# Kernel optimization log

Hardware: AMD Instinct MI355X
Metric: run time of the kernel (lower is better)

Reference implementation:

```python
import jax, jax.numpy as jnp
import numpy as np

Q_CHAN = 8          # q_chan
IN_CHAN = 128
KS = 56             # kernel_size; ks*ks must equal h*w
STRIDE = 2
BN_EPS = 1e-5


def setup_inputs() -> dict:
    key = jax.random.key(0)
    ks = jax.random.split(key, 10)
    n, c, h, w = 4, IN_CHAN, 56, 56
    hw = h * w  # 3136 == KS*KS
    oc = 4 * Q_CHAN  # qkv conv output channels = 32
    return {
        "x": jax.random.normal(ks[0], (n, c, h, w), dtype=jnp.float32),
        # 1x1 conv weight (out_ch, in_ch) and bias
        "w_qkv": jax.random.normal(ks[1], (oc, c), dtype=jnp.float32) * (1.0 / np.sqrt(c)),
        "b_qkv": jnp.zeros((oc,), dtype=jnp.float32),
        # BatchNorm (inference mode) affine + running stats
        "bn_gamma": jnp.ones((oc,), dtype=jnp.float32),
        "bn_beta": jnp.zeros((oc,), dtype=jnp.float32),
        "bn_mean": jnp.zeros((oc,), dtype=jnp.float32),
        "bn_var": jnp.ones((oc,), dtype=jnp.float32),
        # learned relative position biases, trailing dim = ks*ks = h*w
        "rq": jax.random.normal(ks[2], (Q_CHAN, KS * KS), dtype=jnp.float32),
        "rk": jax.random.normal(ks[3], (Q_CHAN, KS * KS), dtype=jnp.float32),
        "rv": jax.random.normal(ks[4], (2 * Q_CHAN, KS * KS), dtype=jnp.float32),
    }


def reference(x, w_qkv, b_qkv, bn_gamma, bn_beta, bn_mean, bn_var, rq, rk, rv):
    n, c, h, w = x.shape
    # 1x1 conv + inference BatchNorm
    qkv = jnp.einsum('nchw,oc->nohw', x, w_qkv) + b_qkv[None, :, None, None]
    scale = bn_gamma / jnp.sqrt(bn_var + BN_EPS)
    qkv = (qkv - bn_mean[None, :, None, None]) * scale[None, :, None, None] + bn_beta[None, :, None, None]
    qkv = qkv.reshape(n, 4 * Q_CHAN, h * w)
    q = qkv[:, :Q_CHAN]            # [n, 8, hw]
    k = qkv[:, Q_CHAN:2 * Q_CHAN]  # [n, 8, hw]
    v = qkv[:, 2 * Q_CHAN:]        # [n, 16, hw]
    # global attention scores with learned positional bias terms: [n, hw, hw]
    sc = (jnp.einsum('nci,ncj->nij', q, k)
          + jnp.einsum('ci,ncj->nij', rq, q)
          + jnp.einsum('ci,ncj->nij', rk, k))
    sc = jax.nn.softmax(sc, axis=2)
    v = v + rv[None]
    out = jnp.einsum('nij,ncj->nci', sc, v).reshape(n, 2 * Q_CHAN, h, w)
    # AvgPool2d(kernel=stride, stride=stride)
    s = STRIDE
    out = out.reshape(n, 2 * Q_CHAN, h // s, s, w // s, s).mean(axis=(3, 5))
    return out
```

## Files before the change

### kernel.cpp

```cpp
#include <hip/hip_runtime.h>

#define HW 3136
#define CIN 128
#define MHAT 40.0f
#define NSEV 7
#define LOG2E 1.44269504088896340736f
#define NEGC  (-57.7078018f)

typedef __attribute__((ext_vector_type(8))) short bf16x8;
typedef __attribute__((ext_vector_type(4))) float f32x4;

__device__ __forceinline__ unsigned cvtpk(float a, float b) {
    unsigned r;
    asm("v_cvt_pk_bf16_f32 %0, %1, %2" : "=v"(r) : "v"(a), "v"(b));
    return r;
}
__device__ __forceinline__ float lo2f(unsigned p) { return __uint_as_float(p << 16); }
__device__ __forceinline__ float hi2f(unsigned p) { return __uint_as_float(p & 0xffff0000u); }
__device__ __forceinline__ float exp2_hw(float x) {
    float r;
    asm("v_exp_f32 %0, %1" : "=v"(r) : "v"(x));
    return r;
}
__device__ __forceinline__ void pl32(unsigned &a, unsigned &b) {
    asm("v_permlane32_swap_b32 %0, %1" : "+v"(a), "+v"(b));
}
__device__ __forceinline__ void pl16(unsigned &a, unsigned &b) {
    asm("v_permlane16_swap_b32 %0, %1" : "+v"(a), "+v"(b));
}

union UF { bf16x8 v; unsigned u[4]; };


__global__ __launch_bounds__(64) void proj_mfma(
    const float* __restrict__ x, const float* __restrict__ w,
    const float* __restrict__ bq, const float* __restrict__ gm,
    const float* __restrict__ bt, const float* __restrict__ mu,
    const float* __restrict__ vr, const float* __restrict__ rq,
    const float* __restrict__ rk, const float* __restrict__ rv,
    short* __restrict__ QKWS, short* __restrict__ ASQB, short* __restrict__ VWS)
{
    const int lane = threadIdx.x;
    const int il = lane & 15, q = lane >> 4;
    const int jb = blockIdx.x * 16;
    const int nn = blockIdx.y;
    const int jA = jb + il;
    const float* xn = x + (size_t)nn * CIN * HW;

    UF xh[4], xl[4];
    #pragma unroll
    for (int s = 0; s < 4; ++s) {
        float xv[8];
        #pragma unroll
        for (int u = 0; u < 8; ++u)
            xv[u] = xn[(size_t)(s * 32 + q * 8 + u) * HW + jA];
        #pragma unroll
        for (int t = 0; t < 4; ++t) {
            unsigned hp = cvtpk(xv[2 * t], xv[2 * t + 1]);
            unsigned lp = cvtpk(xv[2 * t] - lo2f(hp), xv[2 * t + 1] - hi2f(hp));
            xh[s].u[t] = hp;
            xl[s].u[t] = lp;
        }
    }
    UF wh0[4], wl0[4], wh1[4], wl1[4];
    {
        const float* wp0 = w + (size_t)il * CIN;
        const float* wp1 = w + (size_t)(16 + il) * CIN;
        #pragma unroll
        for (int s = 0; s < 4; ++s) {
            float4 f0 = *(const float4*)(wp0 + s * 32 + q * 8);
            float4 f1 = *(const float4*)(wp0 + s * 32 + q * 8 + 4);
            float g0[8] = {f0.x, f0.y, f0.z, f0.w, f1.x, f1.y, f1.z, f1.w};
            float4 h0 = *(const float4*)(wp1 + s * 32 + q * 8);
            float4 h1 = *(const float4*)(wp1 + s * 32 + q * 8 + 4);
            float g1[8] = {h0.x, h0.y, h0.z, h0.w, h1.x, h1.y, h1.z, h1.w};
            #pragma unroll
            for (int t = 0; t < 4; ++t) {
                unsigned hp0 = cvtpk(g0[2 * t], g0[2 * t + 1]);
                unsigned lp0 = cvtpk(g0[2 * t] - lo2f(hp0), g0[2 * t + 1] - hi2f(hp0));
                wh0[s].u[t] = hp0;
                wl0[s].u[t] = lp0;
                unsigned hp1 = cvtpk(g1[2 * t], g1[2 * t + 1]);
                unsigned lp1 = cvtpk(g1[2 * t] - lo2f(hp1), g1[2 * t + 1] - hi2f(hp1));
                wh1[s].u[t] = hp1;
                wl1[s].u[t] = lp1;
            }
        }
    }

    f32x4 a0 = {0.f, 0.f, 0.f, 0.f}, a1 = {0.f, 0.f, 0.f, 0.f};
    #pragma unroll
    for (int s = 0; s < 4; ++s) a0 = __builtin_amdgcn_mfma_f32_16x16x32_bf16(wh0[s].v, xh[s].v, a0, 0, 0, 0);
    #pragma unroll
    for (int s = 0; s < 4; ++s) a1 = __builtin_amdgcn_mfma_f32_16x16x32_bf16(wl0[s].v, xh[s].v, a1, 0, 0, 0);
    #pragma unroll
    for (int s = 0; s < 4; ++s) a1 = __builtin_amdgcn_mfma_f32_16x16x32_bf16(wh0[s].v, xl[s].v, a1, 0, 0, 0);
    const f32x4 d0 = a0 + a1;
    f32x4 b0 = {0.f, 0.f, 0.f, 0.f}, b1 = {0.f, 0.f, 0.f, 0.f};
    #pragma unroll
    for (int s = 0; s < 4; ++s) b0 = __builtin_amdgcn_mfma_f32_16x16x32_bf16(xh[s].v, wh1[s].v, b0, 0, 0, 0);
    #pragma unroll
    for (int s = 0; s < 4; ++s) b1 = __builtin_amdgcn_mfma_f32_16x16x32_bf16(xl[s].v, wh1[s].v, b1, 0, 0, 0);
    #pragma unroll
    for (int s = 0; s < 4; ++s) b1 = __builtin_amdgcn_mfma_f32_16x16x32_bf16(xh[s].v, wl1[s].v, b1, 0, 0, 0);
    const f32x4 d1 = b0 + b1;

    {
        const int jj = jA;
        float hv[4], av[4];
        #pragma unroll
        for (int r = 0; r < 4; ++r) {
            const int ch = q * 4 + r;
            const float sc = gm[ch] * rsqrtf(vr[ch] + 1e-5f);
            const float sh = (bq[ch] - mu[ch]) * sc + bt[ch];
            const float val = d0[r] * sc + sh;
            hv[r] = val;
            const float a = (ch < 8) ? (val + rk[(size_t)ch * HW + jj])
                                     : rq[(size_t)(ch - 8) * HW + jj];
            av[r] = a * LOG2E;
        }
        short* qrow = QKWS + ((size_t)nn * HW + jj) * 32;
        short* arow = ASQB + ((size_t)nn * HW + jj) * 32;
        const int pb = (q * 4) ^ 8;
        unsigned h01 = cvtpk(hv[0], hv[1]), h23 = cvtpk(hv[2], hv[3]);
        unsigned l01 = cvtpk(hv[0] - lo2f(h01), hv[1] - hi2f(h01));
        unsigned l23 = cvtpk(hv[2] - lo2f(h23), hv[3] - hi2f(h23));
        *(unsigned*)&qrow[pb]          = h01;
        *(unsigned*)&qrow[pb + 2]      = h23;
        *(unsigned*)&qrow[16 + pb]     = l01;
        *(unsigned*)&qrow[16 + pb + 2] = l23;
        unsigned c01 = cvtpk(av[0], av[1]), c23 = cvtpk(av[2], av[3]);
        unsigned e01 = cvtpk(av[0] - lo2f(c01), av[1] - hi2f(c01));
        unsigned e23 = cvtpk(av[2] - lo2f(c23), av[3] - hi2f(c23));
        *(unsigned*)&arow[q * 4]          = c01;
        *(unsigned*)&arow[q * 4 + 2]      = c23;
        *(unsigned*)&arow[16 + q * 4]     = e01;
        *(unsigned*)&arow[16 + q * 4 + 2] = e23;
    }
    {
        const int ch = 16 + il;
        const float sc = gm[ch] * rsqrtf(vr[ch] + 1e-5f);
        const float sh = (bq[ch] - mu[ch]) * sc + bt[ch];
        const int jbase = jb + q * 4;
        float4 rvv = *(const float4*)(rv + (size_t)il * HW + jbase);
        float v0 = d1[0] * sc + sh + rvv.x;
        float v1 = d1[1] * sc + sh + rvv.y;
        float v2 = d1[2] * sc + sh + rvv.z;
        float v3 = d1[3] * sc + sh + rvv.w;
        short* vp = VWS + (size_t)(nn * 16 + il) * HW + jbase;
        *(unsigned*)&vp[0] = cvtpk(v0, v1);
        *(unsigned*)&vp[2] = cvtpk(v2, v3);
    }
}

#define JT 224
#define QKS 40
#define VTS 232

__global__ __launch_bounds__(256) void attn_mfma(
    const short* __restrict__ QKWS, const short* __restrict__ ASQB,
    const short* __restrict__ VWS,
    float* __restrict__ ONUM, float* __restrict__ OLS)
{
    __shared__ short QK[JT * QKS + 16];
    __shared__ short VT[16 * VTS];
    const int tid = threadIdx.x;
    const int wv = tid >> 6, lane = tid & 63;
    const int il = lane & 15, q = lane >> 4;
    const int b   = blockIdx.x;
    const int sev = b / 196;
    const int ig  = b % 196;
    const int nn  = ig / 49;
    const int tile = (ig % 49) * 4 + wv;
    const int i0  = tile * 16;

    const bf16x8 bco = *(const bf16x8*)(ASQB + ((size_t)nn * HW + i0 + il) * 32 + q * 8);

    const f32x4 DINIT = {NEGC, NEGC, NEGC, NEGC};
    f32x4 outc = {0.f, 0.f, 0.f, 0.f};
    float lsum = 0.f;

    const int jb0 = (sev * 2 + 0) * JT;
    const int jb1 = (sev * 2 + 1) * JT;
    const int c_v = tid >> 4, jg = tid & 15;

    int4 qa0, qa1, qa2, qa3;
    unsigned vt0, vt1, vt2, vt3, vt4, vt5, vt6;

    if (tid < 8) ((unsigned*)(QK + JT * QKS))[tid] = 0u;

    if (tid < JT) {
        const short* src = QKWS + ((size_t)nn * HW + jb0 + tid) * 32;
        qa0 = *(const int4*)(src);
        qa1 = *(const int4*)(src + 8);
        qa2 = *(const int4*)(src + 16);
        qa3 = *(const int4*)(src + 24);
    }
    {
        const unsigned* vs = (const unsigned*)(VWS + (size_t)(nn * 16 + c_v) * HW + jb0 + jg * 14);
        vt0 = vs[0]; vt1 = vs[1]; vt2 = vs[2]; vt3 = vs[3]; vt4 = vs[4]; vt5 = vs[5]; vt6 = vs[6];
    }
    if (tid < JT) {
        short* row = &QK[tid * QKS];
        *(int4*)&row[0]  = qa0;
        *(int4*)&row[8]  = qa1;
        *(int4*)&row[16] = qa2;
        *(int4*)&row[24] = qa3;
    }
    {
        unsigned* vd = (unsigned*)&VT[c_v * VTS + jg * 14];
        vd[0] = vt0; vd[1] = vt1; vd[2] = vt2; vd[3] = vt3; vd[4] = vt4; vd[5] = vt5; vd[6] = vt6;
    }
    __syncthreads();

    if (tid < JT) {
        const short* src = QKWS + ((size_t)nn * HW + jb1 + tid) * 32;
        qa0 = *(const int4*)(src);
        qa1 = *(const int4*)(src + 8);
        qa2 = *(const int4*)(src + 16);
        qa3 = *(const int4*)(src + 24);
    }
    {
        const unsigned* vs = (const unsigned*)(VWS + (size_t)(nn * 16 + c_v) * HW + jb1 + jg * 14);
        vt0 = vs[0]; vt1 = vs[1]; vt2 = vs[2]; vt3 = vs[3]; vt4 = vs[4]; vt5 = vs[5]; vt6 = vs[6];
    }

    auto compute7 = [&]() {
        const short* zrow = &QK[JT * QKS];
        #pragma unroll
        for (int pr = 0; pr < 7; ++pr) {
            unsigned E0, E1, O0, O1;
            {
                const short* arow = &QK[((2 * pr) * 16 + il) * QKS + (q & 1) * 8];
                bf16x8 a1 = *(const bf16x8*)arow;
                bf16x8 a2 = *(const bf16x8*)((lane < 32) ? arow + 16 : zrow);
                __builtin_amdgcn_s_setprio(1);
                f32x4 d = __builtin_amdgcn_mfma_f32_16x16x32_bf16(a1, bco, DINIT, 0, 0, 0);
                d = __builtin_amdgcn_mfma_f32_16x16x32_bf16(a2, bco, d, 0, 0, 0);
                __builtin_amdgcn_s_setprio(0);
                float p0 = exp2_hw(d[0]), p1 = exp2_hw(d[1]);
                float p2 = exp2_hw(d[2]), p3 = exp2_hw(d[3]);
                lsum += (p0 + p1) + (p2 + p3);
                E0 = cvtpk(p0, p1); E1 = cvtpk(p2, p3);
            }
            {
                const short* arow = &QK[((2 * pr + 1) * 16 + il) * QKS + (q & 1) * 8];
                bf16x8 a1 = *(const bf16x8*)arow;
                bf16x8 a2 = *(const bf16x8*)((lane < 32) ? arow + 16 : zrow);
                __builtin_amdgcn_s_setprio(1);
                f32x4 d = __builtin_amdgcn_mfma_f32_16x16x32_bf16(a1, bco, DINIT, 0, 0, 0);
                d = __builtin_amdgcn_mfma_f32_16x16x32_bf16(a2, bco, d, 0, 0, 0);
                __builtin_amdgcn_s_setprio(0);
                float p0 = exp2_hw(d[0]), p1 = exp2_hw(d[1]);
                float p2 = exp2_hw(d[2]), p3 = exp2_hw(d[3]);
                lsum += (p0 + p1) + (p2 + p3);
                O0 = cvtpk(p0, p1); O1 = cvtpk(p2, p3);
            }
            pl32(E0, O0); pl32(E1, O1);
            pl16(E0, O0); pl16(E1, O1);
            UF ap; ap.u[0] = E0; ap.u[1] = E1; ap.u[2] = O0; ap.u[3] = O1;
            bf16x8 bv = *(const bf16x8*)&VT[il * VTS + pr * 32 + q * 8];
            __builtin_amdgcn_s_setprio(1);
            outc = __builtin_amdgcn_mfma_f32_16x16x32_bf16(ap.v, bv, outc, 0, 0, 0);
            __builtin_amdgcn_s_setprio(0);
        }
    };

    compute7();
    __syncthreads();

    if (tid < JT) {
        short* row = &QK[tid * QKS];
        *(int4*)&row[0]  = qa0;
        *(int4*)&row[8]  = qa1;
        *(int4*)&row[16] = qa2;
        *(int4*)&row[24] = qa3;
    }
    {
        unsigned* vd = (unsigned*)&VT[c_v * VTS + jg * 14];
        vd[0] = vt0; vd[1] = vt1; vd[2] = vt2; vd[3] = vt3; vd[4] = vt4; vd[5] = vt5; vd[6] = vt6;
    }
    __syncthreads();

    compute7();

    lsum += __shfl_xor(lsum, 16);
    lsum += __shfl_xor(lsum, 32);
    float* np = ONUM + ((size_t)(sev * 4 + nn) * 196 + tile) * 256;
    *(f32x4*)(np + il * 16 + q * 4) = outc;
    if (lane < 16)
        OLS[(size_t)(sev * 4 + nn) * HW + i0 + lane] = lsum;
}

__global__ __launch_bounds__(256) void pool_kernel(
    const float* __restrict__ ONUM, const float* __restrict__ OLS,
    float* __restrict__ out)
{
    __shared__ float LI[112];
    __shared__ float PL[2][16][28];
    const int tid = threadIdx.x;
    const int oh  = blockIdx.x;
    const int nn  = blockIdx.y;
    const int T0  = 7 * oh;

    if (tid < 112) {
        float l = 0.f;
        #pragma unroll
        for (int p = 0; p < NSEV; ++p)
            l += OLS[(size_t)(p * 4 + nn) * HW + 112 * oh + tid];
        LI[tid] = l;
    }
    __syncthreads();

    const int c  = tid >> 4;
    const int u0 = tid & 15;
    for (int u = u0; u < 28; u += 16) {
        const int tt = u >> 2, qd = u & 3;
        const int o  = u * 4;
        float4 nu = {0.f, 0.f, 0.f, 0.f};
        #pragma unroll
        for (int p = 0; p < NSEV; ++p) {
            const float4 v = *(const float4*)(ONUM +
                ((size_t)(p * 4 + nn) * 196 + T0 + tt) * 256 + c * 16 + qd * 4);
            nu.x += v.x; nu.y += v.y; nu.z += v.z; nu.w += v.w;
        }
        const float r0 = nu.x / LI[o], r1 = nu.y / LI[o + 1];
        const float r2 = nu.z / LI[o + 2], r3 = nu.w / LI[o + 3];
        const int hb = o / 56, wo = o % 56;
        PL[hb][c][wo >> 1]       = r0 + r1;
        PL[hb][c][(wo >> 1) + 1] = r2 + r3;
    }
    __syncthreads();

    for (int v = tid; v < 448; v += 256) {
        const int cc = v / 28, wo = v % 28;
        out[((nn * 16 + cc) * 28 + oh) * 28 + wo] = 0.25f * (PL[0][cc][wo] + PL[1][cc][wo]);
    }
}

#define FJC 392
#define FPSTR 394

__global__ __launch_bounds__(512, 2) void fused_attn(
    const float* __restrict__ x, const float* __restrict__ w,
    const float* __restrict__ bq, const float* __restrict__ gm,
    const float* __restrict__ bt, const float* __restrict__ mu,
    const float* __restrict__ vr, const float* __restrict__ rq,
    const float* __restrict__ rk, const float* __restrict__ rv,
    float* __restrict__ out)
{
    __shared__ float PT[32][FPSTR];
    __shared__ float SQ[56][16];
    __shared__ float ST[56][17];

    const int tid  = threadIdx.x;
    const int wv   = tid >> 6, lane = tid & 63;
    const int bid  = blockIdx.x;
    const int nn   = bid / 56, rem = bid % 56;
    const int oh   = rem >> 1, half = rem & 1;
    const float* xn = x + (size_t)nn * CIN * HW;

    if (tid < 448) {
        int r = tid >> 3, c = tid & 7;
        int rh = (r >= 28) ? 1 : 0, rw = r - 28*rh;
        int i  = (2*oh + rh)*56 + half*28 + rw;
        float acc = 0.f;
        for (int cc = 0; cc < CIN; ++cc)
            acc += xn[cc*HW + i] * w[c*CIN + cc];
        float s  = gm[c] * rsqrtf(vr[c] + 1e-5f);
        float qv = (acc + bq[c] - mu[c])*s + bt[c];
        SQ[r][c]   = qv + rk[c*HW + i];
        SQ[r][8+c] = rq[c*HW + i];
    }

    float l_[7];
    float ac_[7][16];
    #pragma unroll
    for (int r = 0; r < 7; ++r) {
        l_[r] = 0.f;
        #pragma unroll
        for (int c = 0; c < 16; ++c) ac_[r][c] = 0.f;
    }
    __syncthreads();

    for (int cb = 0; cb < 8; ++cb) {
        const int jbase = cb * FJC;
        const int o0 = wv * 4;
        for (int t = 0; t < 4; ++t) {
            int p = lane + 64*t;
            if (p < 196) {
                int j0 = jbase + 2*p;
                float a0x=0.f,a0y=0.f,a1x=0.f,a1y=0.f,a2x=0.f,a2y=0.f,a3x=0.f,a3y=0.f;
                for (int cc = 0; cc < CIN; ++cc) {
                    float2 xv = *(const float2*)(xn + (size_t)cc*HW + j0);
                    float w0 = w[(o0+0)*CIN + cc];
                    float w1 = w[(o0+1)*CIN + cc];
                    float w2 = w[(o0+2)*CIN + cc];
                    float w3 = w[(o0+3)*CIN + cc];
                    a0x += xv.x*w0; a0y += xv.y*w0;
                    a1x += xv.x*w1; a1y += xv.y*w1;
                    a2x += xv.x*w2; a2y += xv.y*w2;
                    a3x += xv.x*w3; a3y += xv.y*w3;
                }
                #pragma unroll
                for (int u = 0; u < 4; ++u) {
                    int o = o0 + u;
                    float av0 = (u==0)? a0x : (u==1)? a1x : (u==2)? a2x : a3x;
                    float av1 = (u==0)? a0y : (u==1)? a1y : (u==2)? a2y : a3y;
                    float s  = gm[o] * rsqrtf(vr[o] + 1e-5f);
                    float sh = (bq[o] - mu[o])*s + bt[o];
                    float v0 = av0*s + sh, v1 = av1*s + sh;
                    if (o >= 16) {
                        v0 += rv[(o-16)*HW + j0];
                        v1 += rv[(o-16)*HW + j0 + 1];
                    }
                    *(float2*)&PT[o][2*p] = make_float2(v0, v1);
                }
            }
        }
        __syncthreads();

        #pragma unroll
        for (int rr = 0; rr < 7; rr += 2) {
            const bool two = (rr + 1) < 7;
            const int ra = wv*7 + rr;
            float A1a[8], A2a[8], A1b[8], A2b[8];
            #pragma unroll
            for (int c = 0; c < 8; ++c) {
                A1a[c] = SQ[ra][c];   A2a[c] = SQ[ra][8+c];
                A1b[c] = two ? SQ[ra+1][c]   : 0.f;
                A2b[c] = two ? SQ[ra+1][8+c] : 0.f;
            }
            for (int t = 0; t < 7; ++t) {
                int jl = 64*t + lane;
                if (jl < FJC) {
                    float qv[8], kv[8], vv[16];
                    #pragma unroll
                    for (int c = 0; c < 8; ++c) { qv[c] = PT[c][jl]; kv[c] = PT[8+c][jl]; }
                    #pragma unroll
                    for (int c = 0; c < 16; ++c) vv[c] = PT[16+c][jl];
                    float sa = 0.f, sb = 0.f;
                    #pragma unroll
                    for (int c = 0; c < 8; ++c) {
                        sa += A1a[c]*kv[c] + A2a[c]*qv[c];
                        sb += A1b[c]*kv[c] + A2b[c]*qv[c];
                    }
                    float pa = __expf(sa - MHAT);
                    l_[rr] += pa;
                    #pragma unroll
                    for (int c = 0; c < 16; ++c) ac_[rr][c] += pa * vv[c];
                    if (two) {
                        float pb = __expf(sb - MHAT);
                        l_[rr+1] += pb;
                        #pragma unroll
                        for (int c = 0; c < 16; ++c) ac_[rr+1][c] += pb * vv[c];
                    }
                }
            }
        }
        __syncthreads();
    }

    #pragma unroll
    for (int rr = 0; rr < 7; ++rr) {
        int r = wv*7 + rr;
        float l = l_[rr];
        #pragma unroll
        for (int off = 32; off; off >>= 1) l += __shfl_xor(l, off);
        if (lane == 0) ST[r][16] = l;
        #pragma unroll
        for (int c = 0; c < 16; ++c) {
            float a = ac_[rr][c];
            #pragma unroll
            for (int off = 32; off; off >>= 1) a += __shfl_xor(a, off);
            if (lane == c) ST[r][c] = a;
        }
    }
    __syncthreads();

    if (tid < 224) {
        int c = tid & 15, qq = tid >> 4;
        float s = 0.f;
        #pragma unroll
        for (int rh = 0; rh < 2; ++rh)
            #pragma unroll
            for (int dw = 0; dw < 2; ++dw) {
                int r = rh*28 + 2*qq + dw;
                s += ST[r][c] / ST[r][16];
            }
        out[((nn*16 + c)*28 + oh)*28 + half*14 + qq] = 0.25f * s;
    }
}

extern "C" void kernel_launch(void* const* d_in, const int* in_sizes, int n_in,
                              void* d_out, int out_size, void* d_ws, size_t ws_size,
                              hipStream_t stream) {
    const float* x     = (const float*)d_in[0];
    const float* w     = (const float*)d_in[1];
    const float* bq    = (const float*)d_in[2];
    const float* gm    = (const float*)d_in[3];
    const float* bt    = (const float*)d_in[4];
    const float* mu    = (const float*)d_in[5];
    const float* vr    = (const float*)d_in[6];
    const float* rq    = (const float*)d_in[7];
    const float* rk    = (const float*)d_in[8];
    const float* rv    = (const float*)d_in[9];
    float* out = (float*)d_out;

    const size_t ONF = (size_t)NSEV * 4 * 196 * 256;
    const size_t OLF = (size_t)NSEV * 4 * HW;
    const size_t QKF = (size_t)4 * HW * 32;
    const size_t VWF = (size_t)4 * 16 * HW;
    const size_t NEED = (ONF + OLF) * sizeof(float) + (2 * QKF + VWF) * sizeof(short);

    if (ws_size >= NEED) {
        float* ONUM = (float*)d_ws;
        float* OLS  = ONUM + ONF;
        short* QKWS = (short*)(OLS + OLF);
        short* ASQB = QKWS + QKF;
        short* VWS  = ASQB + QKF;
        proj_mfma<<<dim3(196, 4), 64, 0, stream>>>(x, w, bq, gm, bt, mu, vr, rq, rk, rv, QKWS, ASQB, VWS);
        attn_mfma<<<dim3(196 * NSEV), 256, 0, stream>>>(QKWS, ASQB, VWS, ONUM, OLS);
        pool_kernel<<<dim3(28, 4), 256, 0, stream>>>(ONUM, OLS, out);
    } else {
        fused_attn<<<dim3(224), dim3(512), 0, stream>>>(x, w, bq, gm, bt, mu, vr, rq, rk, rv, out);
    }
}
```

Baseline: 97.57 us.

## Split projection K-reduction across two waves and zero B operand instead of LDS zero row

The projection kernel now runs two waves per block, each handling half of the 128-channel reduction, and combines their partial sums through shared memory before one wave writes QK/ASQB and the other writes V. This aims to cut per-wave load latency and register pressure in the memory-bound projection stage. In the attention kernel, the second score MFMA now zeroes the B operand for the upper lanes instead of steering those lanes to a zero row in LDS. That removes a per-iteration select and the zero-row init, at the cost of one extra register vector.

```diff
diff --git a/kernel.cpp b/kernel.cpp
--- a/kernel.cpp
+++ b/kernel.cpp
@@ -32,7 +32,7 @@
 union UF { bf16x8 v; unsigned u[4]; };
 
 
-__global__ __launch_bounds__(64) void proj_mfma(
+__global__ __launch_bounds__(128) void proj_mfma(
     const float* __restrict__ x, const float* __restrict__ w,
     const float* __restrict__ bq, const float* __restrict__ gm,
     const float* __restrict__ bt, const float* __restrict__ mu,
@@ -40,34 +40,40 @@
     const float* __restrict__ rk, const float* __restrict__ rv,
     short* __restrict__ QKWS, short* __restrict__ ASQB, short* __restrict__ VWS)
 {
-    const int lane = threadIdx.x;
+    __shared__ f32x4 XD[2][64];
+    const int tid  = threadIdx.x;
+    const int wv   = tid >> 6;
+    const int lane = tid & 63;
     const int il = lane & 15, q = lane >> 4;
     const int jb = blockIdx.x * 16;
     const int nn = blockIdx.y;
     const int jA = jb + il;
     const float* xn = x + (size_t)nn * CIN * HW;
-
-    UF xh[4], xl[4];
-    #pragma unroll
-    for (int s = 0; s < 4; ++s) {
+    const int s0 = 2 * wv;
+
+    UF xh[2], xl[2];
+    #pragma unroll
+    for (int t = 0; t < 2; ++t) {
+        const int s = s0 + t;
         float xv[8];
         #pragma unroll
         for (int u = 0; u < 8; ++u)
             xv[u] = xn[(size_t)(s * 32 + q * 8 + u) * HW + jA];
         #pragma unroll
-        for (int t = 0; t < 4; ++t) {
-            unsigned hp = cvtpk(xv[2 * t], xv[2 * t + 1]);
-            unsigned lp = cvtpk(xv[2 * t] - lo2f(hp), xv[2 * t + 1] - hi2f(hp));
-            xh[s].u[t] = hp;
-            xl[s].u[t] = lp;
-        }
-    }
-    UF wh0[4], wl0[4], wh1[4], wl1[4];
+        for (int tt = 0; tt < 4; ++tt) {
+            unsigned hp = cvtpk(xv[2 * tt], xv[2 * tt + 1]);
+            unsigned lp = cvtpk(xv[2 * tt] - lo2f(hp), xv[2 * tt + 1] - hi2f(hp));
+            xh[t].u[tt] = hp;
+            xl[t].u[tt] = lp;
+        }
+    }
+    UF wh0[2], wl0[2], wh1[2], wl1[2];
     {
         const float* wp0 = w + (size_t)il * CIN;
         const float* wp1 = w + (size_t)(16 + il) * CIN;
         #pragma unroll
-        for (int s = 0; s < 4; ++s) {
+        for (int t = 0; t < 2; ++t) {
+            const int s = s0 + t;
             float4 f0 = *(const float4*)(wp0 + s * 32 + q * 8);
             float4 f1 = *(const float4*)(wp0 + s * 32 + q * 8 + 4);
             float g0[8] = {f0.x, f0.y, f0.z, f0.w, f1.x, f1.y, f1.z, f1.w};
@@ -75,37 +81,41 @@
             float4 h1 = *(const float4*)(wp1 + s * 32 + q * 8 + 4);
             float g1[8] = {h0.x, h0.y, h0.z, h0.w, h1.x, h1.y, h1.z, h1.w};
             #pragma unroll
-            for (int t = 0; t < 4; ++t) {
-                unsigned hp0 = cvtpk(g0[2 * t], g0[2 * t + 1]);
-                unsigned lp0 = cvtpk(g0[2 * t] - lo2f(hp0), g0[2 * t + 1] - hi2f(hp0));
-                wh0[s].u[t] = hp0;
-                wl0[s].u[t] = lp0;
-                unsigned hp1 = cvtpk(g1[2 * t], g1[2 * t + 1]);
-                unsigned lp1 = cvtpk(g1[2 * t] - lo2f(hp1), g1[2 * t + 1] - hi2f(hp1));
-                wh1[s].u[t] = hp1;
-                wl1[s].u[t] = lp1;
-            }
-        }
-    }
-
-    f32x4 a0 = {0.f, 0.f, 0.f, 0.f}, a1 = {0.f, 0.f, 0.f, 0.f};
-    #pragma unroll
-    for (int s = 0; s < 4; ++s) a0 = __builtin_amdgcn_mfma_f32_16x16x32_bf16(wh0[s].v, xh[s].v, a0, 0, 0, 0);
-    #pragma unroll
-    for (int s = 0; s < 4; ++s) a1 = __builtin_amdgcn_mfma_f32_16x16x32_bf16(wl0[s].v, xh[s].v, a1, 0, 0, 0);
-    #pragma unroll
-    for (int s = 0; s < 4; ++s) a1 = __builtin_amdgcn_mfma_f32_16x16x32_bf16(wh0[s].v, xl[s].v, a1, 0, 0, 0);
-    const f32x4 d0 = a0 + a1;
-    f32x4 b0 = {0.f, 0.f, 0.f, 0.f}, b1 = {0.f, 0.f, 0.f, 0.f};
-    #pragma unroll
-    for (int s = 0; s < 4; ++s) b0 = __builtin_amdgcn_mfma_f32_16x16x32_bf16(xh[s].v, wh1[s].v, b0, 0, 0, 0);
-    #pragma unroll
-    for (int s = 0; s < 4; ++s) b1 = __builtin_amdgcn_mfma_f32_16x16x32_bf16(xl[s].v, wh1[s].v, b1, 0, 0, 0);
-    #pragma unroll
-    for (int s = 0; s < 4; ++s) b1 = __builtin_amdgcn_mfma_f32_16x16x32_bf16(xh[s].v, wl1[s].v, b1, 0, 0, 0);
-    const f32x4 d1 = b0 + b1;
-
-    {
+            for (int tt = 0; tt < 4; ++tt) {
+                unsigned hp0 = cvtpk(g0[2 * tt], g0[2 * tt + 1]);
+                unsigned lp0 = cvtpk(g0[2 * tt] - lo2f(hp0), g0[2 * tt + 1] - hi2f(hp0));
+                wh0[t].u[tt] = hp0;
+                wl0[t].u[tt] = lp0;
+                unsigned hp1 = cvtpk(g1[2 * tt], g1[2 * tt + 1]);
+                unsigned lp1 = cvtpk(g1[2 * tt] - lo2f(hp1), g1[2 * tt + 1] - hi2f(hp1));
+                wh1[t].u[tt] = hp1;
+                wl1[t].u[tt] = lp1;
+            }
+        }
+    }
+
+    const f32x4 zz = {0.f, 0.f, 0.f, 0.f};
+    f32x4 c0 = zz, c1 = zz;
+    #pragma unroll
+    for (int t = 0; t < 2; ++t) c0 = __builtin_amdgcn_mfma_f32_16x16x32_bf16(wh0[t].v, xh[t].v, c0, 0, 0, 0);
+    #pragma unroll
+    for (int t = 0; t < 2; ++t) c1 = __builtin_amdgcn_mfma_f32_16x16x32_bf16(wl0[t].v, xh[t].v, c1, 0, 0, 0);
+    #pragma unroll
+    for (int t = 0; t < 2; ++t) c1 = __builtin_amdgcn_mfma_f32_16x16x32_bf16(wh0[t].v, xl[t].v, c1, 0, 0, 0);
+    f32x4 e0 = zz, e1 = zz;
+    #pragma unroll
+    for (int t = 0; t < 2; ++t) e0 = __builtin_amdgcn_mfma_f32_16x16x32_bf16(xh[t].v, wh1[t].v, e0, 0, 0, 0);
+    #pragma unroll
+    for (int t = 0; t < 2; ++t) e1 = __builtin_amdgcn_mfma_f32_16x16x32_bf16(xl[t].v, wh1[t].v, e1, 0, 0, 0);
+    #pragma unroll
+    for (int t = 0; t < 2; ++t) e1 = __builtin_amdgcn_mfma_f32_16x16x32_bf16(xh[t].v, wl1[t].v, e1, 0, 0, 0);
+
+    if (wv == 1) XD[0][lane] = c0 + c1;
+    else         XD[1][lane] = e0 + e1;
+    __syncthreads();
+
+    if (wv == 0) {
+        const f32x4 d0 = (c0 + c1) + XD[0][lane];
         const int jj = jA;
         float hv[4], av[4];
         #pragma unroll
@@ -136,8 +146,8 @@
         *(unsigned*)&arow[q * 4 + 2]      = c23;
         *(unsigned*)&arow[16 + q * 4]     = e01;
         *(unsigned*)&arow[16 + q * 4 + 2] = e23;
-    }
-    {
+    } else {
+        const f32x4 d1 = (e0 + e1) + XD[1][lane];
         const int ch = 16 + il;
         const float sc = gm[ch] * rsqrtf(vr[ch] + 1e-5f);
         const float sh = (bq[ch] - mu[ch]) * sc + bt[ch];
@@ -162,7 +172,7 @@
     const short* __restrict__ VWS,
     float* __restrict__ ONUM, float* __restrict__ OLS)
 {
-    __shared__ short QK[JT * QKS + 16];
+    __shared__ short QK[JT * QKS];
     __shared__ short VT[16 * VTS];
     const int tid = threadIdx.x;
     const int wv = tid >> 6, lane = tid & 63;
@@ -175,6 +185,8 @@
     const int i0  = tile * 16;
 
     const bf16x8 bco = *(const bf16x8*)(ASQB + ((size_t)nn * HW + i0 + il) * 32 + q * 8);
+    const bf16x8 zero8 = {0, 0, 0, 0, 0, 0, 0, 0};
+    const bf16x8 bco2 = (q < 2) ? bco : zero8;
 
     const f32x4 DINIT = {NEGC, NEGC, NEGC, NEGC};
     f32x4 outc = {0.f, 0.f, 0.f, 0.f};
@@ -186,8 +198,6 @@
 
     int4 qa0, qa1, qa2, qa3;
     unsigned vt0, vt1, vt2, vt3, vt4, vt5, vt6;
-
-    if (tid < 8) ((unsigned*)(QK + JT * QKS))[tid] = 0u;
 
     if (tid < JT) {
         const short* src = QKWS + ((size_t)nn * HW + jb0 + tid) * 32;
@@ -226,17 +236,16 @@
     }
 
     auto compute7 = [&]() {
-        const short* zrow = &QK[JT * QKS];
         #pragma unroll
         for (int pr = 0; pr < 7; ++pr) {
             unsigned E0, E1, O0, O1;
             {
                 const short* arow = &QK[((2 * pr) * 16 + il) * QKS + (q & 1) * 8];
                 bf16x8 a1 = *(const bf16x8*)arow;
-                bf16x8 a2 = *(const bf16x8*)((lane < 32) ? arow + 16 : zrow);
+                bf16x8 a2 = *(const bf16x8*)(arow + 16);
                 __builtin_amdgcn_s_setprio(1);
                 f32x4 d = __builtin_amdgcn_mfma_f32_16x16x32_bf16(a1, bco, DINIT, 0, 0, 0);
-                d = __builtin_amdgcn_mfma_f32_16x16x32_bf16(a2, bco, d, 0, 0, 0);
+                d = __builtin_amdgcn_mfma_f32_16x16x32_bf16(a2, bco2, d, 0, 0, 0);
                 __builtin_amdgcn_s_setprio(0);
                 float p0 = exp2_hw(d[0]), p1 = exp2_hw(d[1]);
                 float p2 = exp2_hw(d[2]), p3 = exp2_hw(d[3]);
@@ -246,10 +255,10 @@
             {
                 const short* arow = &QK[((2 * pr + 1) * 16 + il) * QKS + (q & 1) * 8];
                 bf16x8 a1 = *(const bf16x8*)arow;
-                bf16x8 a2 = *(const bf16x8*)((lane < 32) ? arow + 16 : zrow);
+                bf16x8 a2 = *(const bf16x8*)(arow + 16);
                 __builtin_amdgcn_s_setprio(1);
                 f32x4 d = __builtin_amdgcn_mfma_f32_16x16x32_bf16(a1, bco, DINIT, 0, 0, 0);
-                d = __builtin_amdgcn_mfma_f32_16x16x32_bf16(a2, bco, d, 0, 0, 0);
+                d = __builtin_amdgcn_mfma_f32_16x16x32_bf16(a2, bco2, d, 0, 0, 0);
                 __builtin_amdgcn_s_setprio(0);
                 float p0 = exp2_hw(d[0]), p1 = exp2_hw(d[1]);
                 float p2 = exp2_hw(d[2]), p3 = exp2_hw(d[3]);
@@ -519,7 +528,7 @@
         short* QKWS = (short*)(OLS + OLF);
         short* ASQB = QKWS + QKF;
         short* VWS  = ASQB + QKF;
-        proj_mfma<<<dim3(196, 4), 64, 0, stream>>>(x, w, bq, gm, bt, mu, vr, rq, rk, rv, QKWS, ASQB, VWS);
+        proj_mfma<<<dim3(196, 4), 128, 0, stream>>>(x, w, bq, gm, bt, mu, vr, rq, rk, rv, QKWS, ASQB, VWS);
         attn_mfma<<<dim3(196 * NSEV), 256, 0, stream>>>(QKWS, ASQB, VWS, ONUM, OLS);
         pool_kernel<<<dim3(28, 4), 256, 0, stream>>>(ONUM, OLS, out);
     } else {
```

After: 98.88 us. About the same (+1.3%).
